# Kernel tuning notes

Measured on AMD Instinct MI355X. Metric: run time of the kernel, lower is better.

## Reference

```python
import jax, jax.numpy as jnp
import numpy as np

N_HEAD = 8
N_INPUTS = 2
N_EMBD = 256
B, T1, T2 = 4, 8192, 8192


def setup_inputs() -> dict:
    key = jax.random.key(0)
    ks = jax.random.split(key, 8)
    s = 1.0 / np.sqrt(N_EMBD)
    return {
        "x": jax.random.normal(ks[0], (B, T1, N_EMBD), dtype=jnp.float32),
        "y": jax.random.normal(ks[1], (N_INPUTS, B, T2, N_EMBD), dtype=jnp.float32),
        "Wq": jax.random.normal(ks[2], (N_EMBD, N_EMBD), dtype=jnp.float32) * s,
        "bq": jnp.zeros((N_EMBD,), dtype=jnp.float32),
        "Wk": jax.random.normal(ks[3], (N_INPUTS, N_EMBD, N_EMBD), dtype=jnp.float32) * s,
        "bk": jnp.zeros((N_INPUTS, N_EMBD), dtype=jnp.float32),
        "Wv": jax.random.normal(ks[4], (N_INPUTS, N_EMBD, N_EMBD), dtype=jnp.float32) * s,
        "bv": jnp.zeros((N_INPUTS, N_EMBD), dtype=jnp.float32),
        "Wp": jax.random.normal(ks[5], (N_EMBD, N_EMBD), dtype=jnp.float32) * s,
        "bp": jnp.zeros((N_EMBD,), dtype=jnp.float32),
    }


def _split_heads(t):
    # [B, T, C] -> [B, H, T, d]
    Bt, Tt, C = t.shape
    return t.reshape(Bt, Tt, N_HEAD, C // N_HEAD).transpose(0, 2, 1, 3)


def reference(x, y, Wq, bq, Wk, bk, Wv, bv, Wp, bp):
    Bx, T, C = x.shape
    q = jax.nn.softmax(_split_heads(x @ Wq + bq), axis=-1)  # [B,H,T1,d]
    out = q  # faithful to original: out initialized to q
    for i in range(N_INPUTS):
        k = jax.nn.softmax(_split_heads(y[i] @ Wk[i] + bk[i]), axis=-1)  # [B,H,T2,d]
        v = _split_heads(y[i] @ Wv[i] + bv[i])                            # [B,H,T2,d]
        k_cumsum = k.sum(axis=-2, keepdims=True)                          # [B,H,1,d]
        D_inv = 1.0 / (q * k_cumsum).sum(axis=-1, keepdims=True)          # [B,H,T1,1]
        kv = jnp.einsum('bhtd,bhte->bhde', k, v)                          # [B,H,d,d]
        out = out + jnp.einsum('bhnd,bhde->bhne', q, kv) * D_inv
    # b h n d -> b n (h d)
    out = out.transpose(0, 2, 1, 3).reshape(Bx, T, C)
    return out @ Wp + bp
```

## Files before the change

### kernel.cpp

```cpp
#include <hip/hip_runtime.h>
#include <math.h>

#define NHEAD 8
#define CEMB  256
#define NIN   2
#define BB    4
#define TT    8192

typedef __attribute__((ext_vector_type(8))) short short8;
typedef __attribute__((ext_vector_type(4))) float f32x4;
typedef __attribute__((ext_vector_type(16))) float f32x16;

__device__ __forceinline__ unsigned short f2bf(float f) {
    union { float f; unsigned u; } v; v.f = f;
    unsigned u = v.u;
    return (unsigned short)((u + 0x7fffu + ((u >> 16) & 1u)) >> 16);
}
__device__ __forceinline__ float bf2f(unsigned short s) {
    union { unsigned u; float f; } v; v.u = ((unsigned)s) << 16;
    return v.f;
}

__global__ __launch_bounds__(256) void prep_w(const float* __restrict__ Wq,
    const float* __restrict__ Wk, const float* __restrict__ Wv,
    const float* __restrict__ Wp, unsigned short* __restrict__ wsb)
{
    int gid = blockIdx.x * 256 + threadIdx.x;
    int m = gid >> 16;
    int idx = gid & 65535;
    int n = idx >> 8, k = idx & 255;
    const float* src; unsigned short* dst;
    switch (m) {
        case 0: src = Wq;          dst = wsb;          break;
        case 1: src = Wk;          dst = wsb + 65536;  break;
        case 2: src = Wk + 65536;  dst = wsb + 131072; break;
        case 3: src = Wv;          dst = wsb + 196608; break;
        case 4: src = Wv + 65536;  dst = wsb + 262144; break;
        default: src = Wp;         dst = wsb + 327680; break;
    }
    dst[n * 256 + k] = f2bf(src[k * 256 + n]);
}

template<int ITERS>
__global__ __launch_bounds__(256, 2) void passA(const float* __restrict__ y,
    const float* __restrict__ bk, const float* __restrict__ bv,
    const unsigned short* __restrict__ Wkt, const unsigned short* __restrict__ Wvt,
    float* __restrict__ part)
{
    __shared__ unsigned short ytile[64][256];
    __shared__ unsigned short tr[4][32][64];

    const int i = blockIdx.z, b = blockIdx.y, x0 = blockIdx.x;
    const int tid = threadIdx.x;
    const int wid = tid >> 6, lane = tid & 63;
    const int lg = lane >> 4, li = lane & 15;
    const int l31 = lane & 31, hk = lane >> 5;
    const int h0 = 2 * wid, lm = li & 7;

    float bkb[2][2], bvb[2][2];
    #pragma unroll
    for (int hh = 0; hh < 2; ++hh) {
        bkb[hh][0] = bk[i * CEMB + (h0 + hh) * 32 + li];
        bkb[hh][1] = bk[i * CEMB + (h0 + hh) * 32 + 16 + li];
        bvb[hh][0] = bv[i * CEMB + (h0 + hh) * 32 + li];
        bvb[hh][1] = bv[i * CEMB + (h0 + hh) * 32 + 16 + li];
    }

    f32x16 kvacc0 = {}, kvacc1 = {};
    float ksa0[2] = {0.f, 0.f}, ksa1[2] = {0.f, 0.f};

    #pragma unroll
    for (int iter = 0; iter < ITERS; ++iter) {
        __syncthreads();
        const int row0 = (x0 * ITERS + iter) * 64;
        const float* yb = y + ((size_t)(i * BB + b) * TT + row0) * CEMB;
        #pragma unroll
        for (int j = 0; j < 16; ++j) {
            int idx = tid + j * 256;
            int r = idx >> 6, c4 = (idx & 63) << 2;
            int sw = ((((c4 >> 3) ^ (r & 7)) << 3) | (c4 & 7));
            float4 v4 = *(const float4*)&yb[(size_t)r * CEMB + c4];
            ushort4 p; p.x = f2bf(v4.x); p.y = f2bf(v4.y); p.z = f2bf(v4.z); p.w = f2bf(v4.w);
            *(ushort4*)&ytile[r][sw] = p;
        }
        __syncthreads();

        #pragma unroll
        for (int hh = 0; hh < 2; ++hh) {
            f32x4 acc[4][2];
            #pragma unroll
            for (int rt = 0; rt < 4; ++rt) { acc[rt][0] = (f32x4){}; acc[rt][1] = (f32x4){}; }
            {
                const unsigned short* wk0 = Wkt + ((size_t)(i * 256 + (h0 + hh) * 32 + li)) * 256 + lg * 8;
                const unsigned short* wk1 = wk0 + 16 * 256;
                #pragma unroll 2
                for (int ks = 0; ks < 8; ++ks) {
                    const int sw8 = (((4 * ks + lg) ^ lm) << 3);
                    short8 a0 = *(const short8*)&ytile[li][sw8];
                    short8 a1 = *(const short8*)&ytile[16 + li][sw8];
                    short8 a2 = *(const short8*)&ytile[32 + li][sw8];
                    short8 a3 = *(const short8*)&ytile[48 + li][sw8];
                    short8 f0 = *(const short8*)(wk0 + ks * 32);
                    short8 f1 = *(const short8*)(wk1 + ks * 32);
                    acc[0][0] = __builtin_amdgcn_mfma_f32_16x16x32_bf16(a0, f0, acc[0][0], 0, 0, 0);
                    acc[0][1] = __builtin_amdgcn_mfma_f32_16x16x32_bf16(a0, f1, acc[0][1], 0, 0, 0);
                    acc[1][0] = __builtin_amdgcn_mfma_f32_16x16x32_bf16(a1, f0, acc[1][0], 0, 0, 0);
                    acc[1][1] = __builtin_amdgcn_mfma_f32_16x16x32_bf16(a1, f1, acc[1][1], 0, 0, 0);
                    acc[2][0] = __builtin_amdgcn_mfma_f32_16x16x32_bf16(a2, f0, acc[2][0], 0, 0, 0);
                    acc[2][1] = __builtin_amdgcn_mfma_f32_16x16x32_bf16(a2, f1, acc[2][1], 0, 0, 0);
                    acc[3][0] = __builtin_amdgcn_mfma_f32_16x16x32_bf16(a3, f0, acc[3][0], 0, 0, 0);
                    acc[3][1] = __builtin_amdgcn_mfma_f32_16x16x32_bf16(a3, f1, acc[3][1], 0, 0, 0);
                }
            }
            #pragma unroll
            for (int rt = 0; rt < 4; ++rt) {
                float kq0[4], kq1[4];
                #pragma unroll
                for (int reg = 0; reg < 4; ++reg) {
                    float e0 = __expf(acc[rt][0][reg] + bkb[hh][0]);
                    float e1 = __expf(acc[rt][1][reg] + bkb[hh][1]);
                    float s = e0 + e1;
                    s += __shfl_xor(s, 1, 16);
                    s += __shfl_xor(s, 2, 16);
                    s += __shfl_xor(s, 4, 16);
                    s += __shfl_xor(s, 8, 16);
                    float isv = 1.f / s;
                    kq0[reg] = e0 * isv; kq1[reg] = e1 * isv;
                    ksa0[hh] += kq0[reg]; ksa1[hh] += kq1[reg];
                }
                const int wof = ((((2 * rt + (lg >> 1)) ^ lm) << 3) | ((lg & 1) << 2));
                ushort4 p;
                p.x = f2bf(kq0[0]); p.y = f2bf(kq0[1]); p.z = f2bf(kq0[2]); p.w = f2bf(kq0[3]);
                *(ushort4*)&tr[wid][li][wof] = p;
                p.x = f2bf(kq1[0]); p.y = f2bf(kq1[1]); p.z = f2bf(kq1[2]); p.w = f2bf(kq1[3]);
                *(ushort4*)&tr[wid][16 + li][wof] = p;
            }
            #pragma unroll
            for (int rt = 0; rt < 4; ++rt) { acc[rt][0] = (f32x4){}; acc[rt][1] = (f32x4){}; }
            {
                const unsigned short* wv0 = Wvt + ((size_t)(i * 256 + (h0 + hh) * 32 + li)) * 256 + lg * 8;
                const unsigned short* wv1 = wv0 + 16 * 256;
                #pragma unroll 2
                for (int ks = 0; ks < 8; ++ks) {
                    const int sw8 = (((4 * ks + lg) ^ lm) << 3);
                    short8 a0 = *(const short8*)&ytile[li][sw8];
                    short8 a1 = *(const short8*)&ytile[16 + li][sw8];
                    short8 a2 = *(const short8*)&ytile[32 + li][sw8];
                    short8 a3 = *(const short8*)&ytile[48 + li][sw8];
                    short8 f0 = *(const short8*)(wv0 + ks * 32);
                    short8 f1 = *(const short8*)(wv1 + ks * 32);
                    acc[0][0] = __builtin_amdgcn_mfma_f32_16x16x32_bf16(a0, f0, acc[0][0], 0, 0, 0);
                    acc[0][1] = __builtin_amdgcn_mfma_f32_16x16x32_bf16(a0, f1, acc[0][1], 0, 0, 0);
                    acc[1][0] = __builtin_amdgcn_mfma_f32_16x16x32_bf16(a1, f0, acc[1][0], 0, 0, 0);
                    acc[1][1] = __builtin_amdgcn_mfma_f32_16x16x32_bf16(a1, f1, acc[1][1], 0, 0, 0);
                    acc[2][0] = __builtin_amdgcn_mfma_f32_16x16x32_bf16(a2, f0, acc[2][0], 0, 0, 0);
                    acc[2][1] = __builtin_amdgcn_mfma_f32_16x16x32_bf16(a2, f1, acc[2][1], 0, 0, 0);
                    acc[3][0] = __builtin_amdgcn_mfma_f32_16x16x32_bf16(a3, f0, acc[3][0], 0, 0, 0);
                    acc[3][1] = __builtin_amdgcn_mfma_f32_16x16x32_bf16(a3, f1, acc[3][1], 0, 0, 0);
                }
            }
            asm volatile("s_waitcnt lgkmcnt(0)" ::: "memory");
            short8 ka[4];
            #pragma unroll
            for (int ts = 0; ts < 4; ++ts) {
                const int tof = (((2 * ts + hk) ^ (l31 & 7)) << 3);
                ka[ts] = *(const short8*)&tr[wid][l31][tof];
            }
            asm volatile("s_waitcnt lgkmcnt(0)" ::: "memory");
            #pragma unroll
            for (int rt = 0; rt < 4; ++rt) {
                const int wof = ((((2 * rt + (lg >> 1)) ^ lm) << 3) | ((lg & 1) << 2));
                ushort4 p;
                p.x = f2bf(acc[rt][0][0] + bvb[hh][0]); p.y = f2bf(acc[rt][0][1] + bvb[hh][0]);
                p.z = f2bf(acc[rt][0][2] + bvb[hh][0]); p.w = f2bf(acc[rt][0][3] + bvb[hh][0]);
                *(ushort4*)&tr[wid][li][wof] = p;
                p.x = f2bf(acc[rt][1][0] + bvb[hh][1]); p.y = f2bf(acc[rt][1][1] + bvb[hh][1]);
                p.z = f2bf(acc[rt][1][2] + bvb[hh][1]); p.w = f2bf(acc[rt][1][3] + bvb[hh][1]);
                *(ushort4*)&tr[wid][16 + li][wof] = p;
            }
            asm volatile("s_waitcnt lgkmcnt(0)" ::: "memory");
            #pragma unroll
            for (int ts = 0; ts < 4; ++ts) {
                const int tof = (((2 * ts + hk) ^ (l31 & 7)) << 3);
                short8 vb = *(const short8*)&tr[wid][l31][tof];
                if (hh == 0) kvacc0 = __builtin_amdgcn_mfma_f32_32x32x16_bf16(ka[ts], vb, kvacc0, 0, 0, 0);
                else         kvacc1 = __builtin_amdgcn_mfma_f32_32x32x16_bf16(ka[ts], vb, kvacc1, 0, 0, 0);
            }
        }
    }

    const int slots = TT / (ITERS * 64);
    const size_t slot = (size_t)(i * BB + b) * slots + x0;
    float* pbase = part + slot * (NHEAD * 1056);
    #pragma unroll
    for (int hh = 0; hh < 2; ++hh) {
        float* pb = pbase + (size_t)(h0 + hh) * 1056;
        #pragma unroll
        for (int reg = 0; reg < 16; ++reg) {
            int d = (reg & 3) + 8 * (reg >> 2) + 4 * hk;
            pb[d * 32 + l31] = hh ? kvacc1[reg] : kvacc0[reg];
        }
        float s0 = ksa0[hh], s1 = ksa1[hh];
        s0 += __shfl_xor(s0, 16, 64); s0 += __shfl_xor(s0, 32, 64);
        s1 += __shfl_xor(s1, 16, 64); s1 += __shfl_xor(s1, 32, 64);
        if (lg == 0) { pb[1024 + li] = s0; pb[1024 + 16 + li] = s1; }
    }
}

__global__ __launch_bounds__(256) void reduceKV1(const float* __restrict__ part,
    float* __restrict__ part2, int slots)
{
    const int sc = blockIdx.x, g = blockIdx.y;
    const int ib = g >> 3, h = g & 7;
    const int tid = threadIdx.x;
    const float* p = part + ((size_t)(ib * slots + sc * 8) * NHEAD + h) * 1056;
    float* o = part2 + ((size_t)(sc * 64 + g)) * 1056;
    const size_t sstride = (size_t)NHEAD * 1056;
    for (int e = tid; e < 1056; e += 256) {
        float s = 0.f;
        #pragma unroll
        for (int xx = 0; xx < 8; ++xx) s += p[(size_t)xx * sstride + e];
        o[e] = s;
    }
}

__global__ __launch_bounds__(256) void reduceKV2(const float* __restrict__ part2,
    unsigned short* __restrict__ kvt, float* __restrict__ ksum, int nsc)
{
    const int g = blockIdx.x;
    const int tid = threadIdx.x;
    const size_t gstride = (size_t)64 * 1056;
    const float* p = part2 + (size_t)g * 1056;
    for (int e = tid; e < 1056; e += 256) {
        float s = 0.f;
        for (int sc = 0; sc < nsc; ++sc) s += p[(size_t)sc * gstride + e];
        if (e < 1024) kvt[(size_t)g * 1024 + (e & 31) * 32 + (e >> 5)] = f2bf(s);
        else          ksum[(size_t)g * 32 + (e - 1024)] = s;
    }
}

__global__ __launch_bounds__(512, 4) void passB(const float* __restrict__ x,
    const float* __restrict__ bq, const float* __restrict__ bp,
    const unsigned short* __restrict__ Wqt, const unsigned short* __restrict__ Wpt,
    const unsigned short* __restrict__ kvt, const float* __restrict__ ksum,
    float* __restrict__ out)
{
    __shared__ unsigned short xa[64][256];
    __shared__ unsigned short ql[64][256];
    __shared__ float dl[2][64][8];

    const int b = blockIdx.y, x0 = blockIdx.x;
    const int row0 = x0 * 64;
    const int tid = threadIdx.x;
    const int wid = tid >> 6, lane = tid & 63, lg = lane >> 4, li = lane & 15;
    const int h = wid, lm = li & 7;

    const float* xb = x + ((size_t)b * TT + row0) * CEMB;
    #pragma unroll
    for (int j = 0; j < 8; ++j) {
        int idx = tid + j * 512;
        int r = idx >> 6, c4 = (idx & 63) << 2;
        int sw = ((((c4 >> 3) ^ (r & 7)) << 3) | (c4 & 7));
        float4 v4 = *(const float4*)&xb[(size_t)r * CEMB + c4];
        ushort4 p; p.x = f2bf(v4.x); p.y = f2bf(v4.y); p.z = f2bf(v4.z); p.w = f2bf(v4.w);
        *(ushort4*)&xa[r][sw] = p;
    }
    __syncthreads();

    {
        f32x4 qa[4][2];
        #pragma unroll
        for (int rt = 0; rt < 4; ++rt) { qa[rt][0] = (f32x4){}; qa[rt][1] = (f32x4){}; }

        const unsigned short* wq0 = Wqt + ((size_t)(h * 32 + li)) * 256 + lg * 8;
        const unsigned short* wq1 = wq0 + 16 * 256;
        #pragma unroll 2
        for (int ks = 0; ks < 8; ++ks) {
            const int sw8 = (((4 * ks + lg) ^ lm) << 3);
            short8 a0 = *(const short8*)&xa[li][sw8];
            short8 a1 = *(const short8*)&xa[16 + li][sw8];
            short8 a2 = *(const short8*)&xa[32 + li][sw8];
            short8 a3 = *(const short8*)&xa[48 + li][sw8];
            short8 f0 = *(const short8*)(wq0 + ks * 32);
            short8 f1 = *(const short8*)(wq1 + ks * 32);
            qa[0][0] = __builtin_amdgcn_mfma_f32_16x16x32_bf16(a0, f0, qa[0][0], 0, 0, 0);
            qa[0][1] = __builtin_amdgcn_mfma_f32_16x16x32_bf16(a0, f1, qa[0][1], 0, 0, 0);
            qa[1][0] = __builtin_amdgcn_mfma_f32_16x16x32_bf16(a1, f0, qa[1][0], 0, 0, 0);
            qa[1][1] = __builtin_amdgcn_mfma_f32_16x16x32_bf16(a1, f1, qa[1][1], 0, 0, 0);
            qa[2][0] = __builtin_amdgcn_mfma_f32_16x16x32_bf16(a2, f0, qa[2][0], 0, 0, 0);
            qa[2][1] = __builtin_amdgcn_mfma_f32_16x16x32_bf16(a2, f1, qa[2][1], 0, 0, 0);
            qa[3][0] = __builtin_amdgcn_mfma_f32_16x16x32_bf16(a3, f0, qa[3][0], 0, 0, 0);
            qa[3][1] = __builtin_amdgcn_mfma_f32_16x16x32_bf16(a3, f1, qa[3][1], 0, 0, 0);
        }
        const float bq0 = bq[h * 32 + li];
        const float bq1 = bq[h * 32 + 16 + li];
        #pragma unroll
        for (int rt = 0; rt < 4; ++rt) {
            #pragma unroll
            for (int reg = 0; reg < 4; ++reg) {
                float e0 = __expf(qa[rt][0][reg] + bq0);
                float e1 = __expf(qa[rt][1][reg] + bq1);
                float s = e0 + e1;
                s += __shfl_xor(s, 1, 16);
                s += __shfl_xor(s, 2, 16);
                s += __shfl_xor(s, 4, 16);
                s += __shfl_xor(s, 8, 16);
                float isv = 1.f / s;
                int r = 16 * rt + 4 * lg + reg;
                int r7 = r & 7;
                int sw0 = (((4 * h + (li >> 3)) ^ r7) << 3) | lm;
                int sw1 = (((4 * h + 2 + (li >> 3)) ^ r7) << 3) | lm;
                ql[r][sw0] = f2bf(e0 * isv);
                ql[r][sw1] = f2bf(e1 * isv);
            }
        }
    }
    __syncthreads();

    {
        int r = tid >> 3, hh = tid & 7;
        const float* ks0 = ksum + ((size_t)(0 * BB + b) * 8 + hh) * 32;
        const float* ks1 = ksum + ((size_t)(1 * BB + b) * 8 + hh) * 32;
        float s0 = 0.f, s1 = 0.f;
        #pragma unroll
        for (int d8 = 0; d8 < 4; ++d8) {
            int cu = (((4 * hh + d8) ^ (r & 7)) << 3);
            #pragma unroll
            for (int dd = 0; dd < 8; ++dd) {
                float qv = bf2f(ql[r][cu + dd]);
                s0 += qv * ks0[d8 * 8 + dd];
                s1 += qv * ks1[d8 * 8 + dd];
            }
        }
        dl[0][r][hh] = 1.f / s0;
        dl[1][r][hh] = 1.f / s1;
    }
    __syncthreads();

    #pragma unroll
    for (int rt = 0; rt < 4; ++rt) {
        float of0[4], of1[4];
        #pragma unroll
        for (int reg = 0; reg < 4; ++reg) {
            int rk = (4 * lg + reg) & 7;
            int r = 16 * rt + 4 * lg + reg;
            int col0 = (((4 * h + (li >> 3)) ^ rk) << 3) | lm;
            int col1 = (((4 * h + 2 + (li >> 3)) ^ rk) << 3) | lm;
            of0[reg] = bf2f(ql[r][col0]);
            of1[reg] = bf2f(ql[r][col1]);
        }
        short8 af = *(const short8*)&ql[16 * rt + li][(((4 * h + lg) ^ lm) << 3)];
        #pragma unroll
        for (int ii = 0; ii < NIN; ++ii) {
            const unsigned short* kvb = kvt + ((size_t)((ii * BB + b) * 8 + h)) * 1024;
            short8 b0 = *(const short8*)(kvb + (size_t)li * 32 + lg * 8);
            short8 b1 = *(const short8*)(kvb + (size_t)(16 + li) * 32 + lg * 8);
            f32x4 z = {};
            f32x4 t0 = __builtin_amdgcn_mfma_f32_16x16x32_bf16(af, b0, z, 0, 0, 0);
            f32x4 t1 = __builtin_amdgcn_mfma_f32_16x16x32_bf16(af, b1, z, 0, 0, 0);
            #pragma unroll
            for (int reg = 0; reg < 4; ++reg) {
                float dv = dl[ii][16 * rt + 4 * lg + reg][h];
                of0[reg] += t0[reg] * dv;
                of1[reg] += t1[reg] * dv;
            }
        }
        #pragma unroll
        for (int reg = 0; reg < 4; ++reg) {
            int rk = (4 * lg + reg) & 7;
            int r = 16 * rt + 4 * lg + reg;
            int col0 = (((4 * h + (li >> 3)) ^ rk) << 3) | lm;
            int col1 = (((4 * h + 2 + (li >> 3)) ^ rk) << 3) | lm;
            xa[r][col0] = f2bf(of0[reg]);
            xa[r][col1] = f2bf(of1[reg]);
        }
    }
    __syncthreads();

    {
        f32x4 of[4][2];
        #pragma unroll
        for (int rt = 0; rt < 4; ++rt) { of[rt][0] = (f32x4){}; of[rt][1] = (f32x4){}; }
        const unsigned short* wp0 = Wpt + ((size_t)(h * 32 + li)) * 256 + lg * 8;
        const unsigned short* wp1 = wp0 + 16 * 256;
        #pragma unroll 2
        for (int ks = 0; ks < 8; ++ks) {
            const int sw8 = (((4 * ks + lg) ^ lm) << 3);
            short8 a0 = *(const short8*)&xa[li][sw8];
            short8 a1 = *(const short8*)&xa[16 + li][sw8];
            short8 a2 = *(const short8*)&xa[32 + li][sw8];
            short8 a3 = *(const short8*)&xa[48 + li][sw8];
            short8 f0 = *(const short8*)(wp0 + ks * 32);
            short8 f1 = *(const short8*)(wp1 + ks * 32);
            of[0][0] = __builtin_amdgcn_mfma_f32_16x16x32_bf16(a0, f0, of[0][0], 0, 0, 0);
            of[0][1] = __builtin_amdgcn_mfma_f32_16x16x32_bf16(a0, f1, of[0][1], 0, 0, 0);
            of[1][0] = __builtin_amdgcn_mfma_f32_16x16x32_bf16(a1, f0, of[1][0], 0, 0, 0);
            of[1][1] = __builtin_amdgcn_mfma_f32_16x16x32_bf16(a1, f1, of[1][1], 0, 0, 0);
            of[2][0] = __builtin_amdgcn_mfma_f32_16x16x32_bf16(a2, f0, of[2][0], 0, 0, 0);
            of[2][1] = __builtin_amdgcn_mfma_f32_16x16x32_bf16(a2, f1, of[2][1], 0, 0, 0);
            of[3][0] = __builtin_amdgcn_mfma_f32_16x16x32_bf16(a3, f0, of[3][0], 0, 0, 0);
            of[3][1] = __builtin_amdgcn_mfma_f32_16x16x32_bf16(a3, f1, of[3][1], 0, 0, 0);
        }
        const float bp0 = bp[h * 32 + li];
        const float bp1 = bp[h * 32 + 16 + li];
        #pragma unroll
        for (int rt = 0; rt < 4; ++rt) {
            #pragma unroll
            for (int reg = 0; reg < 4; ++reg) {
                int r = 16 * rt + 4 * lg + reg;
                float* ob = out + ((size_t)b * TT + row0 + r) * CEMB + h * 32;
                ob[li]      = of[rt][0][reg] + bp0;
                ob[16 + li] = of[rt][1][reg] + bp1;
            }
        }
    }
}

extern "C" void kernel_launch(void* const* d_in, const int* in_sizes, int n_in,
                              void* d_out, int out_size, void* d_ws, size_t ws_size,
                              hipStream_t stream)
{
    const float* x  = (const float*)d_in[0];
    const float* y  = (const float*)d_in[1];
    const float* Wq = (const float*)d_in[2];
    const float* bq = (const float*)d_in[3];
    const float* Wk = (const float*)d_in[4];
    const float* bk = (const float*)d_in[5];
    const float* Wv = (const float*)d_in[6];
    const float* bv = (const float*)d_in[7];
    const float* Wp = (const float*)d_in[8];
    const float* bp = (const float*)d_in[9];
    float* out = (float*)d_out;

    const size_t wbytes = 786432;
    int slots = 128;
    size_t partBytes  = (size_t)NIN * BB * slots * NHEAD * 1056 * 4;
    size_t part2Bytes = (size_t)(slots / 8) * 64 * 1056 * 4;
    if (wbytes + partBytes + part2Bytes + 131072 + 8192 > ws_size) {
        slots = 64;
        partBytes  = (size_t)NIN * BB * slots * NHEAD * 1056 * 4;
        part2Bytes = (size_t)(slots / 8) * 64 * 1056 * 4;
    }
    unsigned short* wsb = (unsigned short*)d_ws;
    float* part  = (float*)((char*)d_ws + wbytes);
    float* part2 = (float*)((char*)d_ws + wbytes + partBytes);
    unsigned short* kvt = (unsigned short*)((char*)d_ws + wbytes + partBytes + part2Bytes);
    float* ksum = (float*)((char*)d_ws + wbytes + partBytes + part2Bytes + 131072);

    hipLaunchKernelGGL(prep_w, dim3(1536), dim3(256), 0, stream, Wq, Wk, Wv, Wp, wsb);
    if (slots == 128)
        hipLaunchKernelGGL((passA<1>), dim3(128, BB, NIN), dim3(256), 0, stream,
                           y, bk, bv, wsb + 65536, wsb + 196608, part);
    else
        hipLaunchKernelGGL((passA<2>), dim3(64, BB, NIN), dim3(256), 0, stream,
                           y, bk, bv, wsb + 65536, wsb + 196608, part);
    hipLaunchKernelGGL(reduceKV1, dim3(slots / 8, 64), dim3(256), 0, stream, part, part2, slots);
    hipLaunchKernelGGL(reduceKV2, dim3(64), dim3(256), 0, stream, part2, kvt, ksum, slots / 8);
    hipLaunchKernelGGL(passB, dim3(128, BB), dim3(512), 0, stream,
                       x, bq, bp, wsb + 0, wsb + 327680, kvt, ksum, out);
}
```

Before: 123.5 us.

## Use one wave per head in passA with 512-thread blocks and padded transpose tile

passA now launches 512 threads (8 waves) per block, one wave per head, instead of 4 waves each looping over two heads. The transpose scratch buffer goes from an XOR swizzle to row padding (68 columns), and the y tile load is split across twice as many threads. The goal is more parallelism per block and shorter per-wave critical paths, at the cost of more LDS per block and possibly lower occupancy under the 512x2 launch bounds. Padding replaces the swizzle, which could change bank-conflict behaviour.

After: 119.5 us. 1.03x faster.

```diff
diff --git a/kernel.cpp b/kernel.cpp
--- a/kernel.cpp
+++ b/kernel.cpp
@@ -42,32 +42,33 @@
 }
 
 template<int ITERS>
-__global__ __launch_bounds__(256, 2) void passA(const float* __restrict__ y,
+__global__ __launch_bounds__(512, 2) void passA(const float* __restrict__ y,
     const float* __restrict__ bk, const float* __restrict__ bv,
     const unsigned short* __restrict__ Wkt, const unsigned short* __restrict__ Wvt,
     float* __restrict__ part)
 {
     __shared__ unsigned short ytile[64][256];
-    __shared__ unsigned short tr[4][32][64];
+    __shared__ unsigned short tr[8][32][68];
 
     const int i = blockIdx.z, b = blockIdx.y, x0 = blockIdx.x;
     const int tid = threadIdx.x;
     const int wid = tid >> 6, lane = tid & 63;
     const int lg = lane >> 4, li = lane & 15;
     const int l31 = lane & 31, hk = lane >> 5;
-    const int h0 = 2 * wid, lm = li & 7;
-
-    float bkb[2][2], bvb[2][2];
-    #pragma unroll
-    for (int hh = 0; hh < 2; ++hh) {
-        bkb[hh][0] = bk[i * CEMB + (h0 + hh) * 32 + li];
-        bkb[hh][1] = bk[i * CEMB + (h0 + hh) * 32 + 16 + li];
-        bvb[hh][0] = bv[i * CEMB + (h0 + hh) * 32 + li];
-        bvb[hh][1] = bv[i * CEMB + (h0 + hh) * 32 + 16 + li];
-    }
-
-    f32x16 kvacc0 = {}, kvacc1 = {};
-    float ksa0[2] = {0.f, 0.f}, ksa1[2] = {0.f, 0.f};
+    const int h = wid, lm = li & 7;
+
+    const float bk0 = bk[i * CEMB + h * 32 + li];
+    const float bk1 = bk[i * CEMB + h * 32 + 16 + li];
+    const float bv0 = bv[i * CEMB + h * 32 + li];
+    const float bv1 = bv[i * CEMB + h * 32 + 16 + li];
+
+    const unsigned short* wk0 = Wkt + ((size_t)(i * 256 + h * 32 + li)) * 256 + lg * 8;
+    const unsigned short* wk1 = wk0 + 16 * 256;
+    const unsigned short* wv0 = Wvt + ((size_t)(i * 256 + h * 32 + li)) * 256 + lg * 8;
+    const unsigned short* wv1 = wv0 + 16 * 256;
+
+    f32x16 kvacc = {};
+    float ksa0 = 0.f, ksa1 = 0.f;
 
     #pragma unroll
     for (int iter = 0; iter < ITERS; ++iter) {
@@ -75,8 +76,8 @@
         const int row0 = (x0 * ITERS + iter) * 64;
         const float* yb = y + ((size_t)(i * BB + b) * TT + row0) * CEMB;
         #pragma unroll
-        for (int j = 0; j < 16; ++j) {
-            int idx = tid + j * 256;
+        for (int j = 0; j < 8; ++j) {
+            int idx = tid + j * 512;
             int r = idx >> 6, c4 = (idx & 63) << 2;
             int sw = ((((c4 >> 3) ^ (r & 7)) << 3) | (c4 & 7));
             float4 v4 = *(const float4*)&yb[(size_t)r * CEMB + c4];
@@ -85,126 +86,106 @@
         }
         __syncthreads();
 
-        #pragma unroll
-        for (int hh = 0; hh < 2; ++hh) {
-            f32x4 acc[4][2];
+        f32x4 acc[4][2];
+        #pragma unroll
+        for (int rt = 0; rt < 4; ++rt) { acc[rt][0] = (f32x4){}; acc[rt][1] = (f32x4){}; }
+        #pragma unroll 2
+        for (int ks = 0; ks < 8; ++ks) {
+            const int sw8 = (((4 * ks + lg) ^ lm) << 3);
+            short8 a0 = *(const short8*)&ytile[li][sw8];
+            short8 a1 = *(const short8*)&ytile[16 + li][sw8];
+            short8 a2 = *(const short8*)&ytile[32 + li][sw8];
+            short8 a3 = *(const short8*)&ytile[48 + li][sw8];
+            short8 f0 = *(const short8*)(wk0 + ks * 32);
+            short8 f1 = *(const short8*)(wk1 + ks * 32);
+            acc[0][0] = __builtin_amdgcn_mfma_f32_16x16x32_bf16(a0, f0, acc[0][0], 0, 0, 0);
+            acc[0][1] = __builtin_amdgcn_mfma_f32_16x16x32_bf16(a0, f1, acc[0][1], 0, 0, 0);
+            acc[1][0] = __builtin_amdgcn_mfma_f32_16x16x32_bf16(a1, f0, acc[1][0], 0, 0, 0);
+            acc[1][1] = __builtin_amdgcn_mfma_f32_16x16x32_bf16(a1, f1, acc[1][1], 0, 0, 0);
+            acc[2][0] = __builtin_amdgcn_mfma_f32_16x16x32_bf16(a2, f0, acc[2][0], 0, 0, 0);
+            acc[2][1] = __builtin_amdgcn_mfma_f32_16x16x32_bf16(a2, f1, acc[2][1], 0, 0, 0);
+            acc[3][0] = __builtin_amdgcn_mfma_f32_16x16x32_bf16(a3, f0, acc[3][0], 0, 0, 0);
+            acc[3][1] = __builtin_amdgcn_mfma_f32_16x16x32_bf16(a3, f1, acc[3][1], 0, 0, 0);
+        }
+        #pragma unroll
+        for (int rt = 0; rt < 4; ++rt) {
+            float kq0[4], kq1[4];
             #pragma unroll
-            for (int rt = 0; rt < 4; ++rt) { acc[rt][0] = (f32x4){}; acc[rt][1] = (f32x4){}; }
-            {
-                const unsigned short* wk0 = Wkt + ((size_t)(i * 256 + (h0 + hh) * 32 + li)) * 256 + lg * 8;
-                const unsigned short* wk1 = wk0 + 16 * 256;
-                #pragma unroll 2
-                for (int ks = 0; ks < 8; ++ks) {
-                    const int sw8 = (((4 * ks + lg) ^ lm) << 3);
-                    short8 a0 = *(const short8*)&ytile[li][sw8];
-                    short8 a1 = *(const short8*)&ytile[16 + li][sw8];
-                    short8 a2 = *(const short8*)&ytile[32 + li][sw8];
-                    short8 a3 = *(const short8*)&ytile[48 + li][sw8];
-                    short8 f0 = *(const short8*)(wk0 + ks * 32);
-                    short8 f1 = *(const short8*)(wk1 + ks * 32);
-                    acc[0][0] = __builtin_amdgcn_mfma_f32_16x16x32_bf16(a0, f0, acc[0][0], 0, 0, 0);
-                    acc[0][1] = __builtin_amdgcn_mfma_f32_16x16x32_bf16(a0, f1, acc[0][1], 0, 0, 0);
-                    acc[1][0] = __builtin_amdgcn_mfma_f32_16x16x32_bf16(a1, f0, acc[1][0], 0, 0, 0);
-                    acc[1][1] = __builtin_amdgcn_mfma_f32_16x16x32_bf16(a1, f1, acc[1][1], 0, 0, 0);
-                    acc[2][0] = __builtin_amdgcn_mfma_f32_16x16x32_bf16(a2, f0, acc[2][0], 0, 0, 0);
-                    acc[2][1] = __builtin_amdgcn_mfma_f32_16x16x32_bf16(a2, f1, acc[2][1], 0, 0, 0);
-                    acc[3][0] = __builtin_amdgcn_mfma_f32_16x16x32_bf16(a3, f0, acc[3][0], 0, 0, 0);
-                    acc[3][1] = __builtin_amdgcn_mfma_f32_16x16x32_bf16(a3, f1, acc[3][1], 0, 0, 0);
-                }
+            for (int reg = 0; reg < 4; ++reg) {
+                float e0 = __expf(acc[rt][0][reg] + bk0);
+                float e1 = __expf(acc[rt][1][reg] + bk1);
+                float s = e0 + e1;
+                s += __shfl_xor(s, 1, 16);
+                s += __shfl_xor(s, 2, 16);
+                s += __shfl_xor(s, 4, 16);
+                s += __shfl_xor(s, 8, 16);
+                float isv = 1.f / s;
+                kq0[reg] = e0 * isv; kq1[reg] = e1 * isv;
+                ksa0 += kq0[reg]; ksa1 += kq1[reg];
             }
-            #pragma unroll
-            for (int rt = 0; rt < 4; ++rt) {
-                float kq0[4], kq1[4];
-                #pragma unroll
-                for (int reg = 0; reg < 4; ++reg) {
-                    float e0 = __expf(acc[rt][0][reg] + bkb[hh][0]);
-                    float e1 = __expf(acc[rt][1][reg] + bkb[hh][1]);
-                    float s = e0 + e1;
-                    s += __shfl_xor(s, 1, 16);
-                    s += __shfl_xor(s, 2, 16);
-                    s += __shfl_xor(s, 4, 16);
-                    s += __shfl_xor(s, 8, 16);
-                    float isv = 1.f / s;
-                    kq0[reg] = e0 * isv; kq1[reg] = e1 * isv;
-                    ksa0[hh] += kq0[reg]; ksa1[hh] += kq1[reg];
-                }
-                const int wof = ((((2 * rt + (lg >> 1)) ^ lm) << 3) | ((lg & 1) << 2));
-                ushort4 p;
-                p.x = f2bf(kq0[0]); p.y = f2bf(kq0[1]); p.z = f2bf(kq0[2]); p.w = f2bf(kq0[3]);
-                *(ushort4*)&tr[wid][li][wof] = p;
-                p.x = f2bf(kq1[0]); p.y = f2bf(kq1[1]); p.z = f2bf(kq1[2]); p.w = f2bf(kq1[3]);
-                *(ushort4*)&tr[wid][16 + li][wof] = p;
-            }
-            #pragma unroll
-            for (int rt = 0; rt < 4; ++rt) { acc[rt][0] = (f32x4){}; acc[rt][1] = (f32x4){}; }
-            {
-                const unsigned short* wv0 = Wvt + ((size_t)(i * 256 + (h0 + hh) * 32 + li)) * 256 + lg * 8;
-                const unsigned short* wv1 = wv0 + 16 * 256;
-                #pragma unroll 2
-                for (int ks = 0; ks < 8; ++ks) {
-                    const int sw8 = (((4 * ks + lg) ^ lm) << 3);
-                    short8 a0 = *(const short8*)&ytile[li][sw8];
-                    short8 a1 = *(const short8*)&ytile[16 + li][sw8];
-                    short8 a2 = *(const short8*)&ytile[32 + li][sw8];
-                    short8 a3 = *(const short8*)&ytile[48 + li][sw8];
-                    short8 f0 = *(const short8*)(wv0 + ks * 32);
-                    short8 f1 = *(const short8*)(wv1 + ks * 32);
-                    acc[0][0] = __builtin_amdgcn_mfma_f32_16x16x32_bf16(a0, f0, acc[0][0], 0, 0, 0);
-                    acc[0][1] = __builtin_amdgcn_mfma_f32_16x16x32_bf16(a0, f1, acc[0][1], 0, 0, 0);
-                    acc[1][0] = __builtin_amdgcn_mfma_f32_16x16x32_bf16(a1, f0, acc[1][0], 0, 0, 0);
-                    acc[1][1] = __builtin_amdgcn_mfma_f32_16x16x32_bf16(a1, f1, acc[1][1], 0, 0, 0);
-                    acc[2][0] = __builtin_amdgcn_mfma_f32_16x16x32_bf16(a2, f0, acc[2][0], 0, 0, 0);
-                    acc[2][1] = __builtin_amdgcn_mfma_f32_16x16x32_bf16(a2, f1, acc[2][1], 0, 0, 0);
-                    acc[3][0] = __builtin_amdgcn_mfma_f32_16x16x32_bf16(a3, f0, acc[3][0], 0, 0, 0);
-                    acc[3][1] = __builtin_amdgcn_mfma_f32_16x16x32_bf16(a3, f1, acc[3][1], 0, 0, 0);
-                }
-            }
-            asm volatile("s_waitcnt lgkmcnt(0)" ::: "memory");
-            short8 ka[4];
-            #pragma unroll
-            for (int ts = 0; ts < 4; ++ts) {
-                const int tof = (((2 * ts + hk) ^ (l31 & 7)) << 3);
-                ka[ts] = *(const short8*)&tr[wid][l31][tof];
-            }
-            asm volatile("s_waitcnt lgkmcnt(0)" ::: "memory");
-            #pragma unroll
-            for (int rt = 0; rt < 4; ++rt) {
-                const int wof = ((((2 * rt + (lg >> 1)) ^ lm) << 3) | ((lg & 1) << 2));
-                ushort4 p;
-                p.x = f2bf(acc[rt][0][0] + bvb[hh][0]); p.y = f2bf(acc[rt][0][1] + bvb[hh][0]);
-                p.z = f2bf(acc[rt][0][2] + bvb[hh][0]); p.w = f2bf(acc[rt][0][3] + bvb[hh][0]);
-                *(ushort4*)&tr[wid][li][wof] = p;
-                p.x = f2bf(acc[rt][1][0] + bvb[hh][1]); p.y = f2bf(acc[rt][1][1] + bvb[hh][1]);
-                p.z = f2bf(acc[rt][1][2] + bvb[hh][1]); p.w = f2bf(acc[rt][1][3] + bvb[hh][1]);
-                *(ushort4*)&tr[wid][16 + li][wof] = p;
-            }
-            asm volatile("s_waitcnt lgkmcnt(0)" ::: "memory");
-            #pragma unroll
-            for (int ts = 0; ts < 4; ++ts) {
-                const int tof = (((2 * ts + hk) ^ (l31 & 7)) << 3);
-                short8 vb = *(const short8*)&tr[wid][l31][tof];
-                if (hh == 0) kvacc0 = __builtin_amdgcn_mfma_f32_32x32x16_bf16(ka[ts], vb, kvacc0, 0, 0, 0);
-                else         kvacc1 = __builtin_amdgcn_mfma_f32_32x32x16_bf16(ka[ts], vb, kvacc1, 0, 0, 0);
-            }
-        }
+            ushort4 p;
+            p.x = f2bf(kq0[0]); p.y = f2bf(kq0[1]); p.z = f2bf(kq0[2]); p.w = f2bf(kq0[3]);
+            *(ushort4*)&tr[wid][li][16 * rt + 4 * lg] = p;
+            p.x = f2bf(kq1[0]); p.y = f2bf(kq1[1]); p.z = f2bf(kq1[2]); p.w = f2bf(kq1[3]);
+            *(ushort4*)&tr[wid][16 + li][16 * rt + 4 * lg] = p;
+        }
+        #pragma unroll
+        for (int rt = 0; rt < 4; ++rt) { acc[rt][0] = (f32x4){}; acc[rt][1] = (f32x4){}; }
+        #pragma unroll 2
+        for (int ks = 0; ks < 8; ++ks) {
+            const int sw8 = (((4 * ks + lg) ^ lm) << 3);
+            short8 a0 = *(const short8*)&ytile[li][sw8];
+            short8 a1 = *(const short8*)&ytile[16 + li][sw8];
+            short8 a2 = *(const short8*)&ytile[32 + li][sw8];
+            short8 a3 = *(const short8*)&ytile[48 + li][sw8];
+            short8 f0 = *(const short8*)(wv0 + ks * 32);
+            short8 f1 = *(const short8*)(wv1 + ks * 32);
+            acc[0][0] = __builtin_amdgcn_mfma_f32_16x16x32_bf16(a0, f0, acc[0][0], 0, 0, 0);
+            acc[0][1] = __builtin_amdgcn_mfma_f32_16x16x32_bf16(a0, f1, acc[0][1], 0, 0, 0);
+            acc[1][0] = __builtin_amdgcn_mfma_f32_16x16x32_bf16(a1, f0, acc[1][0], 0, 0, 0);
+            acc[1][1] = __builtin_amdgcn_mfma_f32_16x16x32_bf16(a1, f1, acc[1][1], 0, 0, 0);
+            acc[2][0] = __builtin_amdgcn_mfma_f32_16x16x32_bf16(a2, f0, acc[2][0], 0, 0, 0);
+            acc[2][1] = __builtin_amdgcn_mfma_f32_16x16x32_bf16(a2, f1, acc[2][1], 0, 0, 0);
+            acc[3][0] = __builtin_amdgcn_mfma_f32_16x16x32_bf16(a3, f0, acc[3][0], 0, 0, 0);
+            acc[3][1] = __builtin_amdgcn_mfma_f32_16x16x32_bf16(a3, f1, acc[3][1], 0, 0, 0);
+        }
+        asm volatile("s_waitcnt lgkmcnt(0)" ::: "memory");
+        short8 ka[4];
+        #pragma unroll
+        for (int ts = 0; ts < 4; ++ts)
+            ka[ts] = *(const short8*)&tr[wid][l31][ts * 16 + hk * 8];
+        asm volatile("s_waitcnt lgkmcnt(0)" ::: "memory");
+        #pragma unroll
+        for (int rt = 0; rt < 4; ++rt) {
+            ushort4 p;
+            p.x = f2bf(acc[rt][0][0] + bv0); p.y = f2bf(acc[rt][0][1] + bv0);
+            p.z = f2bf(acc[rt][0][2] + bv0); p.w = f2bf(acc[rt][0][3] + bv0);
+            *(ushort4*)&tr[wid][li][16 * rt + 4 * lg] = p;
+            p.x = f2bf(acc[rt][1][0] + bv1); p.y = f2bf(acc[rt][1][1] + bv1);
+            p.z = f2bf(acc[rt][1][2] + bv1); p.w = f2bf(acc[rt][1][3] + bv1);
+            *(ushort4*)&tr[wid][16 + li][16 * rt + 4 * lg] = p;
+        }
+        asm volatile("s_waitcnt lgkmcnt(0)" ::: "memory");
+        #pragma unroll
+        for (int ts = 0; ts < 4; ++ts) {
+            short8 vb = *(const short8*)&tr[wid][l31][ts * 16 + hk * 8];
+            kvacc = __builtin_amdgcn_mfma_f32_32x32x16_bf16(ka[ts], vb, kvacc, 0, 0, 0);
+        }
+        asm volatile("s_waitcnt lgkmcnt(0)" ::: "memory");
     }
 
     const int slots = TT / (ITERS * 64);
     const size_t slot = (size_t)(i * BB + b) * slots + x0;
-    float* pbase = part + slot * (NHEAD * 1056);
+    float* pb = part + slot * (NHEAD * 1056) + (size_t)h * 1056;
     #pragma unroll
-    for (int hh = 0; hh < 2; ++hh) {
-        float* pb = pbase + (size_t)(h0 + hh) * 1056;
-        #pragma unroll
-        for (int reg = 0; reg < 16; ++reg) {
-            int d = (reg & 3) + 8 * (reg >> 2) + 4 * hk;
-            pb[d * 32 + l31] = hh ? kvacc1[reg] : kvacc0[reg];
-        }
-        float s0 = ksa0[hh], s1 = ksa1[hh];
-        s0 += __shfl_xor(s0, 16, 64); s0 += __shfl_xor(s0, 32, 64);
-        s1 += __shfl_xor(s1, 16, 64); s1 += __shfl_xor(s1, 32, 64);
-        if (lg == 0) { pb[1024 + li] = s0; pb[1024 + 16 + li] = s1; }
-    }
+    for (int reg = 0; reg < 16; ++reg) {
+        int d = (reg & 3) + 8 * (reg >> 2) + 4 * hk;
+        pb[d * 32 + l31] = kvacc[reg];
+    }
+    float s0 = ksa0, s1 = ksa1;
+    s0 += __shfl_xor(s0, 16, 64); s0 += __shfl_xor(s0, 32, 64);
+    s1 += __shfl_xor(s1, 16, 64); s1 += __shfl_xor(s1, 32, 64);
+    if (lg == 0) { pb[1024 + li] = s0; pb[1024 + 16 + li] = s1; }
 }
 
 __global__ __launch_bounds__(256) void reduceKV1(const float* __restrict__ part,
@@ -449,10 +430,10 @@
 
     hipLaunchKernelGGL(prep_w, dim3(1536), dim3(256), 0, stream, Wq, Wk, Wv, Wp, wsb);
     if (slots == 128)
-        hipLaunchKernelGGL((passA<1>), dim3(128, BB, NIN), dim3(256), 0, stream,
+        hipLaunchKernelGGL((passA<1>), dim3(128, BB, NIN), dim3(512), 0, stream,
                            y, bk, bv, wsb + 65536, wsb + 196608, part);
     else
-        hipLaunchKernelGGL((passA<2>), dim3(64, BB, NIN), dim3(256), 0, stream,
+        hipLaunchKernelGGL((passA<2>), dim3(64, BB, NIN), dim3(512), 0, stream,
                            y, bk, bv, wsb + 65536, wsb + 196608, part);
     hipLaunchKernelGGL(reduceKV1, dim3(slots / 8, 64), dim3(256), 0, stream, part, part2, slots);
     hipLaunchKernelGGL(reduceKV2, dim3(64), dim3(256), 0, stream, part2, kvt, ksum, slots / 8);
```
